# Kernel tuning notes

Measured on AMD Instinct MI355X. Metric: run time of the kernel, lower is better.

Reference implementation:

```python
import jax, jax.numpy as jnp
import numpy as np


def rotary_pos_emb(x):
    # x: [b, h, l, k]; interleaved rotary embedding (pairs are (0,1),(2,3),...)
    dim = x.shape[-1]
    seq = x.shape[-2]
    ts = jnp.arange(0, dim, 2, dtype=jnp.float32)
    inv_freqs = 10000.0 ** (-ts / dim)                      # [dim/2]
    grid = jnp.arange(seq, dtype=jnp.float32)[:, None] * inv_freqs[None, :]  # [l, dim/2]
    sin_embs = jnp.repeat(jnp.sin(grid), 2, axis=-1)[None]  # [1, l, dim] (interleaved repeat)
    cos_embs = jnp.repeat(jnp.cos(grid), 2, axis=-1)[None]
    x1, x2 = x[..., ::2], x[..., 1::2]
    xs = jnp.stack([-x2, x1], axis=-1).reshape(x.shape)     # interleave (-x2, x1)
    return x * cos_embs + xs * sin_embs


def setup_inputs() -> dict:
    key = jax.random.key(0)
    ks = jax.random.split(key, 5)
    b, l, d = 2, 2048, 1024
    scale = 1.0 / np.sqrt(d)
    return {
        "x": jax.random.normal(ks[0], (b, l, d), dtype=jnp.float32),
        "Wq": jax.random.normal(ks[1], (d, d), dtype=jnp.float32) * scale,
        "Wk": jax.random.normal(ks[2], (d, d), dtype=jnp.float32) * scale,
        "Wv": jax.random.normal(ks[3], (d, d), dtype=jnp.float32) * scale,
        "Wo": jax.random.normal(ks[4], (d, d), dtype=jnp.float32) * scale,
        "is_training": 0,
    }


def reference(x, Wq, Wk, Wv, Wo, is_training):
    n_heads = 16
    b, l, d = x.shape
    k_size = d // n_heads
    # NOTE: module scales q by 1/sqrt(model_size), not 1/sqrt(key_size)
    q = (x @ Wq) / jnp.sqrt(jnp.float32(d))
    q = q.reshape(b, l, n_heads, k_size).transpose(0, 2, 1, 3)  # b h l k
    k = (x @ Wk).reshape(b, l, n_heads, k_size).transpose(0, 2, 1, 3)
    v = (x @ Wv).reshape(b, l, n_heads, k_size).transpose(0, 2, 1, 3)
    q = rotary_pos_emb(q)
    k = rotary_pos_emb(k)
    logits = jnp.einsum('bhik,bhjk->bhij', q, k)  # no mask, no dropout (eval)
    a = jax.nn.softmax(logits, axis=-1)
    y = jnp.einsum('bhij,bhjv->bhiv', a, v)
    y = y.transpose(0, 2, 1, 3).reshape(b, l, d)  # b l (h v)
    return y @ Wo
```

## Files before the change

### kernel.cpp

```cpp
#include <hip/hip_runtime.h>
#include <stdint.h>

typedef unsigned short u16;
using short8 = __attribute__((ext_vector_type(8))) short;
using f32x4  = __attribute__((ext_vector_type(4))) float;

typedef __attribute__((address_space(1))) unsigned int gu32;
typedef __attribute__((address_space(3))) unsigned int lu32;

__device__ __forceinline__ void gl2lds16(const u16* g, u16* lds_wave_base) {
    __builtin_amdgcn_global_load_lds(
        (gu32*)(uintptr_t)(const void*)g,
        (lu32*)(uint32_t)(uintptr_t)(void*)lds_wave_base,
        16, 0, 0);
}

__device__ inline float bf2f(u16 u) {
    union { unsigned int i; float f; } v;
    v.i = ((unsigned int)u) << 16;
    return v.f;
}
__device__ inline u16 f2bf(float f) {
    union { float f; unsigned int i; } v;
    v.f = f;
    unsigned int x = v.i;
    return (u16)((x + 0x7fffu + ((x >> 16) & 1u)) >> 16);
}
__device__ inline u16 f2bf_trunc(float f) {
    union { float f; unsigned int i; } v;
    v.f = f;
    return (u16)(v.i >> 16);
}

__global__ __launch_bounds__(256) void cvt_x(const float* __restrict__ x,
                                             u16* __restrict__ xb)
{
    int i = (blockIdx.x * 256 + threadIdx.x) * 4;
    float4 v = *(const float4*)(x + i);
    ushort4 o;
    o.x = f2bf(v.x); o.y = f2bf(v.y); o.z = f2bf(v.z); o.w = f2bf(v.w);
    *(ushort4*)(xb + i) = o;
}

__global__ __launch_bounds__(256) void rope_tab(float2* __restrict__ tab)
{
    int idx = blockIdx.x * 256 + threadIdx.x;
    int pos = idx >> 5, pi = idx & 31;
    const float l2_10000_over_32 = 0.41524101186f;
    float ang = (float)pos * __builtin_amdgcn_exp2f(-(float)pi * l2_10000_over_32);
    float sn, cs;
    __sincosf(ang, &sn, &cs);
    tab[idx] = make_float2(cs, sn);
}

__global__ __launch_bounds__(256) void transpose4_cvt(
    const float* __restrict__ w0, const float* __restrict__ w1,
    const float* __restrict__ w2, const float* __restrict__ w3,
    u16* __restrict__ t0, u16* __restrict__ t1,
    u16* __restrict__ t2, u16* __restrict__ t3)
{
    __shared__ u16 tile[32][33];
    const float* src; u16* dst;
    switch (blockIdx.z) {
        case 0:  src = w0; dst = t0; break;
        case 1:  src = w1; dst = t1; break;
        case 2:  src = w2; dst = t2; break;
        default: src = w3; dst = t3; break;
    }
    int tx = threadIdx.x, ty = threadIdx.y;
    int c0 = blockIdx.x * 32, r0 = blockIdx.y * 32;
    #pragma unroll
    for (int i = 0; i < 4; i++)
        tile[ty + i * 8][tx] = f2bf(src[(size_t)(r0 + ty + i * 8) * 1024 + c0 + tx]);
    __syncthreads();
    #pragma unroll
    for (int i = 0; i < 4; i++)
        dst[(size_t)(c0 + ty + i * 8) * 1024 + r0 + tx] = tile[tx][ty + i * 8];
}

__global__ __launch_bounds__(256) void transpose_v(const u16* __restrict__ Vb,
                                                   u16* __restrict__ VT)
{
    __shared__ u16 t[32][33];
    int bh = blockIdx.z, b = bh >> 4, h = bh & 15;
    int p0 = blockIdx.x * 32, c0 = blockIdx.y * 32;
    int tx = threadIdx.x, ty = threadIdx.y;
    #pragma unroll
    for (int i = 0; i < 4; i++)
        t[ty + i * 8][tx] = Vb[(size_t)(b * 2048 + p0 + ty + i * 8) * 1024 + h * 64 + c0 + tx];
    __syncthreads();
    #pragma unroll
    for (int i = 0; i < 4; i++)
        VT[((size_t)bh * 64 + c0 + ty + i * 8) * 2048 + p0 + tx] = t[tx][ty + i * 8];
}

__global__ __launch_bounds__(256) void gemm_qkv(
    const u16* __restrict__ A, const u16* __restrict__ Bt,
    const float2* __restrict__ ropetab,
    u16* __restrict__ Qb, u16* __restrict__ Kb, u16* __restrict__ Vb)
{
    __shared__ __align__(16) u16 As[128 * 32];
    __shared__ __align__(16) u16 Bs[128 * 32];
    __shared__ float2 scs[128 * 33];

    const int tid  = threadIdx.x;
    const int lane = tid & 63;
    const int wid  = tid >> 6;
    const int quad = lane >> 4;
    const int l15  = lane & 15;
    const int wm   = wid >> 1, wn = wid & 1;

    const int m0 = blockIdx.y * 128;
    const int n0 = blockIdx.x * 128;
    const int mat = n0 >> 10;
    const int ln0 = n0 & 1023;
    u16* C = (mat == 0) ? Qb : (mat == 1 ? Kb : Vb);

    if (mat < 2) {
        int pos0 = m0 & 2047;
        #pragma unroll
        for (int t = 0; t < 16; t++) {
            int idx = t * 256 + tid;
            int rr = idx >> 5, pp = idx & 31;
            scs[rr * 33 + pp] = ropetab[(size_t)(pos0 + rr) * 32 + pp];
        }
    }

    f32x4 acc[4][4] = {};

    for (int k0 = 0; k0 < 1024; k0 += 32) {
        #pragma unroll
        for (int it = 0; it < 2; it++) {
            int c   = it * 256 + tid;
            int row = c >> 2;
            int col = ((c & 3) ^ (row & 3)) * 8;
            u16* lbA = &As[(size_t)(it * 256 + wid * 64) * 8];
            u16* lbB = &Bs[(size_t)(it * 256 + wid * 64) * 8];
            gl2lds16(&A [(size_t)(m0 + row) * 1024 + k0 + col], lbA);
            gl2lds16(&Bt[(size_t)(n0 + row) * 1024 + k0 + col], lbB);
        }
        __syncthreads();

        short8 a[4], b[4];
        #pragma unroll
        for (int i = 0; i < 4; i++) {
            int ra = wm * 64 + i * 16 + l15;
            int rb = wn * 64 + i * 16 + l15;
            a[i] = *(const short8*)(&As[ra * 32 + ((quad ^ (ra & 3)) * 8)]);
            b[i] = *(const short8*)(&Bs[rb * 32 + ((quad ^ (rb & 3)) * 8)]);
        }
        #pragma unroll
        for (int i = 0; i < 4; i++)
            #pragma unroll
            for (int j = 0; j < 4; j++)
                acc[i][j] = __builtin_amdgcn_mfma_f32_16x16x32_bf16(a[i], b[j], acc[i][j], 0, 0, 0);
        __syncthreads();
    }

    const float scale = (mat == 0) ? (0.03125f * 1.44269504f) : 1.0f;
    const bool do_rope = (mat < 2);
    const int odd = l15 & 1;

    #pragma unroll
    for (int i = 0; i < 4; i++)
        #pragma unroll
        for (int j = 0; j < 4; j++)
            #pragma unroll
            for (int r = 0; r < 4; r++) {
                int lrow = wm * 64 + i * 16 + quad * 4 + r;
                int col  = ln0 + wn * 64 + j * 16 + l15;
                float v = acc[i][j][r] * scale;
                float outv;
                if (do_rope) {
                    float vp = __shfl_xor(v, 1);
                    int pi   = (col & 63) >> 1;
                    float2 sc = scs[lrow * 33 + pi];
                    outv = odd ? (v * sc.x + vp * sc.y) : (v * sc.x - vp * sc.y);
                } else {
                    outv = v;
                }
                C[(size_t)(m0 + lrow) * 1024 + col] = f2bf(outv);
            }
}

__global__ __launch_bounds__(256) void gemm_out(
    const u16* __restrict__ A, const u16* __restrict__ Bt, float* __restrict__ C)
{
    __shared__ __align__(16) u16 As[128 * 32];
    __shared__ __align__(16) u16 Bs[128 * 32];

    const int tid  = threadIdx.x;
    const int lane = tid & 63;
    const int wid  = tid >> 6;
    const int quad = lane >> 4;
    const int l15  = lane & 15;
    const int wm   = wid >> 1, wn = wid & 1;

    const int m0 = blockIdx.y * 128;
    const int n0 = blockIdx.x * 128;

    f32x4 acc[4][4] = {};

    for (int k0 = 0; k0 < 1024; k0 += 32) {
        #pragma unroll
        for (int it = 0; it < 2; it++) {
            int c   = it * 256 + tid;
            int row = c >> 2;
            int col = ((c & 3) ^ (row & 3)) * 8;
            u16* lbA = &As[(size_t)(it * 256 + wid * 64) * 8];
            u16* lbB = &Bs[(size_t)(it * 256 + wid * 64) * 8];
            gl2lds16(&A [(size_t)(m0 + row) * 1024 + k0 + col], lbA);
            gl2lds16(&Bt[(size_t)(n0 + row) * 1024 + k0 + col], lbB);
        }
        __syncthreads();

        short8 a[4], b[4];
        #pragma unroll
        for (int i = 0; i < 4; i++) {
            int ra = wm * 64 + i * 16 + l15;
            int rb = wn * 64 + i * 16 + l15;
            a[i] = *(const short8*)(&As[ra * 32 + ((quad ^ (ra & 3)) * 8)]);
            b[i] = *(const short8*)(&Bs[rb * 32 + ((quad ^ (rb & 3)) * 8)]);
        }
        #pragma unroll
        for (int i = 0; i < 4; i++)
            #pragma unroll
            for (int j = 0; j < 4; j++)
                acc[i][j] = __builtin_amdgcn_mfma_f32_16x16x32_bf16(a[i], b[j], acc[i][j], 0, 0, 0);
        __syncthreads();
    }

    #pragma unroll
    for (int i = 0; i < 4; i++)
        #pragma unroll
        for (int j = 0; j < 4; j++)
            #pragma unroll
            for (int r = 0; r < 4; r++) {
                int row = m0 + wm * 64 + i * 16 + quad * 4 + r;
                int col = n0 + wn * 64 + j * 16 + l15;
                C[(size_t)row * 1024 + col] = acc[i][j][r];
            }
}

__global__ __launch_bounds__(512) void attn(
    const u16* __restrict__ Q, const u16* __restrict__ Kb,
    const u16* __restrict__ VT, u16* __restrict__ Y)
{
    __shared__ __align__(16) u16 Ks [128 * 64];
    __shared__ __align__(16) u16 VTs[64 * 128];
    __shared__ __align__(16) u16 Ps [8][16 * 64];

    const int tid  = threadIdx.x;
    const int lane = tid & 63, wid = tid >> 6;
    const int quad = lane >> 4, l15 = lane & 15;

    const int bh = blockIdx.x;
    const int qt = blockIdx.y;
    const int bb = bh >> 4, h = bh & 15;

    const size_t base = ((size_t)bb * 2048) * 1024 + (size_t)h * 64;

    short8 qf[2];
    {
        size_t qrow = (size_t)qt * 128 + wid * 16 + l15;
        const u16* qp = Q + base + qrow * 1024;
        qf[0] = *(const short8*)(qp + quad * 8);
        qf[1] = *(const short8*)(qp + 32 + quad * 8);
    }

    f32x4 o[4] = {};
    float l_r[4] = {0.f, 0.f, 0.f, 0.f};

    for (int j0 = 0; j0 < 2048; j0 += 128) {
        __syncthreads();
        #pragma unroll
        for (int it = 0; it < 2; it++) {
            int c = it * 512 + tid;
            int rk = c >> 3, ck = ((c & 7)  ^ (rk & 7))  * 8;
            int rv = c >> 4, cv = ((c & 15) ^ (rv & 15)) * 8;
            u16* lbK = &Ks [(size_t)(it * 512 + wid * 64) * 8];
            u16* lbV = &VTs[(size_t)(it * 512 + wid * 64) * 8];
            gl2lds16(&Kb[base + (size_t)(j0 + rk) * 1024 + ck], lbK);
            gl2lds16(&VT[((size_t)bh * 64 + rv) * 2048 + j0 + cv], lbV);
        }
        __syncthreads();

        f32x4 s[8];
        #pragma unroll
        for (int nt = 0; nt < 8; nt++) {
            int R = nt * 16 + l15;
            short8 k0 = *(const short8*)(&Ks[R * 64 + (( quad      ^ (R & 7)) * 8)]);
            short8 k1 = *(const short8*)(&Ks[R * 64 + (((quad + 4) ^ (R & 7)) * 8)]);
            f32x4 z = {};
            z = __builtin_amdgcn_mfma_f32_16x16x32_bf16(qf[0], k0, z, 0, 0, 0);
            z = __builtin_amdgcn_mfma_f32_16x16x32_bf16(qf[1], k1, z, 0, 0, 0);
            s[nt] = z;
        }

        #pragma unroll
        for (int hh = 0; hh < 2; hh++) {
            #pragma unroll
            for (int n4 = 0; n4 < 4; n4++) {
                int nt = hh * 4 + n4;
                #pragma unroll
                for (int r = 0; r < 4; r++) {
                    float p = __builtin_amdgcn_exp2f(s[nt][r]);
                    l_r[r] += p;
                    int m = quad * 4 + r;
                    int col = n4 * 16 + l15;
                    Ps[wid][m * 64 + (((col >> 3) ^ (m & 7)) * 8) + (col & 7)]
                        = f2bf_trunc(p);
                }
            }
            asm volatile("s_waitcnt lgkmcnt(0)" ::: "memory");

            short8 pa0 = *(const short8*)(&Ps[wid][l15 * 64 + (( quad      ^ (l15 & 7)) * 8)]);
            short8 pa1 = *(const short8*)(&Ps[wid][l15 * 64 + (((quad + 4) ^ (l15 & 7)) * 8)]);
            #pragma unroll
            for (int nt = 0; nt < 4; nt++) {
                int R = nt * 16 + l15;
                short8 vb0 = *(const short8*)(&VTs[R * 128 + (((hh * 8 + quad)     ^ (R & 15)) * 8)]);
                short8 vb1 = *(const short8*)(&VTs[R * 128 + (((hh * 8 + quad + 4) ^ (R & 15)) * 8)]);
                o[nt] = __builtin_amdgcn_mfma_f32_16x16x32_bf16(pa0, vb0, o[nt], 0, 0, 0);
                o[nt] = __builtin_amdgcn_mfma_f32_16x16x32_bf16(pa1, vb1, o[nt], 0, 0, 0);
            }
            asm volatile("" ::: "memory");
        }
    }

    #pragma unroll
    for (int r = 0; r < 4; r++) {
        l_r[r] += __shfl_xor(l_r[r], 1);
        l_r[r] += __shfl_xor(l_r[r], 2);
        l_r[r] += __shfl_xor(l_r[r], 4);
        l_r[r] += __shfl_xor(l_r[r], 8);
        l_r[r] = 1.0f / l_r[r];
    }

    size_t qrow0 = (size_t)qt * 128 + wid * 16;
    #pragma unroll
    for (int nt = 0; nt < 4; nt++)
        #pragma unroll
        for (int r = 0; r < 4; r++) {
            size_t row = qrow0 + quad * 4 + r;
            Y[base + row * 1024 + nt * 16 + l15] = f2bf(o[nt][r] * l_r[r]);
        }
}

extern "C" void kernel_launch(void* const* d_in, const int* in_sizes, int n_in,
                              void* d_out, int out_size, void* d_ws, size_t ws_size,
                              hipStream_t stream)
{
    const float* x  = (const float*)d_in[0];
    const float* Wq = (const float*)d_in[1];
    const float* Wk = (const float*)d_in[2];
    const float* Wv = (const float*)d_in[3];
    const float* Wo = (const float*)d_in[4];
    float* out = (float*)d_out;

    char* ws = (char*)d_ws;
    u16*    xb    = (u16*)   (ws + (0ull  << 20));
    u16*    WqkvT = (u16*)   (ws + (8ull  << 20));
    u16*    WoT   = (u16*)   (ws + (14ull << 20));
    u16*    Qb    = (u16*)   (ws + (16ull << 20));
    u16*    Kb    = (u16*)   (ws + (24ull << 20));
    u16*    Vb    = (u16*)   (ws + (32ull << 20));
    u16*    VTb   = (u16*)   (ws + (40ull << 20));
    u16*    Yb    = (u16*)   (ws + (48ull << 20));
    float2* tab   = (float2*)(ws + (56ull << 20));

    cvt_x<<<4096, 256, 0, stream>>>(x, xb);
    rope_tab<<<256, 256, 0, stream>>>(tab);
    transpose4_cvt<<<dim3(32, 32, 4), dim3(32, 8), 0, stream>>>(
        Wq, Wk, Wv, Wo,
        WqkvT, WqkvT + (1024ull * 1024), WqkvT + (2048ull * 1024), WoT);
    gemm_qkv<<<dim3(24, 32), 256, 0, stream>>>(xb, WqkvT, tab, Qb, Kb, Vb);
    transpose_v<<<dim3(64, 2, 32), dim3(32, 8), 0, stream>>>(Vb, VTb);
    attn<<<dim3(32, 16), 512, 0, stream>>>(Qb, Kb, VTb, Yb);
    gemm_out<<<dim3(8, 32), 256, 0, stream>>>(Yb, WoT, out);
}
```

Baseline: 205.8 us.

## Give each attention wave two query tiles and fold rope table into transpose

The attention kernel drops from 8 waves to 4 waves per block. Each wave now handles 32 query rows, so every K and V fragment read from LDS feeds two MFMAs, which halves LDS read traffic per FLOP but doubles the accumulator registers per wave. Separately, the rope sin/cos table is now computed inside the weight transpose kernel as an extra grid slice, which removes one kernel launch. The risk is lower occupancy and less latency hiding in attention.

```diff
diff --git a/kernel.cpp b/kernel.cpp
--- a/kernel.cpp
+++ b/kernel.cpp
@@ -42,23 +42,27 @@
     *(ushort4*)(xb + i) = o;
 }
 
-__global__ __launch_bounds__(256) void rope_tab(float2* __restrict__ tab)
-{
-    int idx = blockIdx.x * 256 + threadIdx.x;
-    int pos = idx >> 5, pi = idx & 31;
-    const float l2_10000_over_32 = 0.41524101186f;
-    float ang = (float)pos * __builtin_amdgcn_exp2f(-(float)pi * l2_10000_over_32);
-    float sn, cs;
-    __sincosf(ang, &sn, &cs);
-    tab[idx] = make_float2(cs, sn);
-}
-
 __global__ __launch_bounds__(256) void transpose4_cvt(
     const float* __restrict__ w0, const float* __restrict__ w1,
     const float* __restrict__ w2, const float* __restrict__ w3,
     u16* __restrict__ t0, u16* __restrict__ t1,
-    u16* __restrict__ t2, u16* __restrict__ t3)
-{
+    u16* __restrict__ t2, u16* __restrict__ t3,
+    float2* __restrict__ tab)
+{
+    int tx = threadIdx.x, ty = threadIdx.y;
+    if (blockIdx.z == 4) {
+        int idx = (blockIdx.y * 32 + blockIdx.x) * 256 + ty * 32 + tx;
+        if (idx < 65536) {
+            int pos = idx >> 5, pi = idx & 31;
+            const float l2_10000_over_32 = 0.41524101186f;
+            float ang = (float)pos *
+                __builtin_amdgcn_exp2f(-(float)pi * l2_10000_over_32);
+            float sn, cs;
+            __sincosf(ang, &sn, &cs);
+            tab[idx] = make_float2(cs, sn);
+        }
+        return;
+    }
     __shared__ u16 tile[32][33];
     const float* src; u16* dst;
     switch (blockIdx.z) {
@@ -67,7 +71,6 @@
         case 2:  src = w2; dst = t2; break;
         default: src = w3; dst = t3; break;
     }
-    int tx = threadIdx.x, ty = threadIdx.y;
     int c0 = blockIdx.x * 32, r0 = blockIdx.y * 32;
     #pragma unroll
     for (int i = 0; i < 4; i++)
@@ -242,7 +245,7 @@
             }
 }
 
-__global__ __launch_bounds__(512) void attn(
+__global__ __launch_bounds__(256) void attn(
     const u16* __restrict__ Q, const u16* __restrict__ Kb,
     const u16* __restrict__ VT, u16* __restrict__ Y)
 {
@@ -260,91 +263,110 @@
 
     const size_t base = ((size_t)bb * 2048) * 1024 + (size_t)h * 64;
 
-    short8 qf[2];
-    {
-        size_t qrow = (size_t)qt * 128 + wid * 16 + l15;
+    short8 qf[2][2];
+    #pragma unroll
+    for (int mi = 0; mi < 2; mi++) {
+        size_t qrow = (size_t)qt * 128 + wid * 32 + mi * 16 + l15;
         const u16* qp = Q + base + qrow * 1024;
-        qf[0] = *(const short8*)(qp + quad * 8);
-        qf[1] = *(const short8*)(qp + 32 + quad * 8);
-    }
-
-    f32x4 o[4] = {};
-    float l_r[4] = {0.f, 0.f, 0.f, 0.f};
+        qf[mi][0] = *(const short8*)(qp + quad * 8);
+        qf[mi][1] = *(const short8*)(qp + 32 + quad * 8);
+    }
+
+    f32x4 o[2][4] = {};
+    float l_r[2][4] = {};
 
     for (int j0 = 0; j0 < 2048; j0 += 128) {
         __syncthreads();
         #pragma unroll
-        for (int it = 0; it < 2; it++) {
-            int c = it * 512 + tid;
+        for (int it = 0; it < 4; it++) {
+            int c = it * 256 + tid;
             int rk = c >> 3, ck = ((c & 7)  ^ (rk & 7))  * 8;
             int rv = c >> 4, cv = ((c & 15) ^ (rv & 15)) * 8;
-            u16* lbK = &Ks [(size_t)(it * 512 + wid * 64) * 8];
-            u16* lbV = &VTs[(size_t)(it * 512 + wid * 64) * 8];
+            u16* lbK = &Ks [(size_t)(it * 256 + wid * 64) * 8];
+            u16* lbV = &VTs[(size_t)(it * 256 + wid * 64) * 8];
             gl2lds16(&Kb[base + (size_t)(j0 + rk) * 1024 + ck], lbK);
             gl2lds16(&VT[((size_t)bh * 64 + rv) * 2048 + j0 + cv], lbV);
         }
         __syncthreads();
 
-        f32x4 s[8];
+        f32x4 s[2][8];
         #pragma unroll
         for (int nt = 0; nt < 8; nt++) {
             int R = nt * 16 + l15;
             short8 k0 = *(const short8*)(&Ks[R * 64 + (( quad      ^ (R & 7)) * 8)]);
             short8 k1 = *(const short8*)(&Ks[R * 64 + (((quad + 4) ^ (R & 7)) * 8)]);
-            f32x4 z = {};
-            z = __builtin_amdgcn_mfma_f32_16x16x32_bf16(qf[0], k0, z, 0, 0, 0);
-            z = __builtin_amdgcn_mfma_f32_16x16x32_bf16(qf[1], k1, z, 0, 0, 0);
-            s[nt] = z;
+            #pragma unroll
+            for (int mi = 0; mi < 2; mi++) {
+                f32x4 z = {};
+                z = __builtin_amdgcn_mfma_f32_16x16x32_bf16(qf[mi][0], k0, z, 0, 0, 0);
+                z = __builtin_amdgcn_mfma_f32_16x16x32_bf16(qf[mi][1], k1, z, 0, 0, 0);
+                s[mi][nt] = z;
+            }
         }
 
         #pragma unroll
         for (int hh = 0; hh < 2; hh++) {
             #pragma unroll
-            for (int n4 = 0; n4 < 4; n4++) {
-                int nt = hh * 4 + n4;
+            for (int mi = 0; mi < 2; mi++)
                 #pragma unroll
-                for (int r = 0; r < 4; r++) {
-                    float p = __builtin_amdgcn_exp2f(s[nt][r]);
-                    l_r[r] += p;
-                    int m = quad * 4 + r;
-                    int col = n4 * 16 + l15;
-                    Ps[wid][m * 64 + (((col >> 3) ^ (m & 7)) * 8) + (col & 7)]
-                        = f2bf_trunc(p);
+                for (int n4 = 0; n4 < 4; n4++) {
+                    int nt = hh * 4 + n4;
+                    #pragma unroll
+                    for (int r = 0; r < 4; r++) {
+                        float p = __builtin_amdgcn_exp2f(s[mi][nt][r]);
+                        l_r[mi][r] += p;
+                        int m = quad * 4 + r;
+                        int col = n4 * 16 + l15;
+                        Ps[wid * 2 + mi][m * 64 + (((col >> 3) ^ (m & 7)) * 8) + (col & 7)]
+                            = f2bf_trunc(p);
+                    }
                 }
-            }
             asm volatile("s_waitcnt lgkmcnt(0)" ::: "memory");
 
-            short8 pa0 = *(const short8*)(&Ps[wid][l15 * 64 + (( quad      ^ (l15 & 7)) * 8)]);
-            short8 pa1 = *(const short8*)(&Ps[wid][l15 * 64 + (((quad + 4) ^ (l15 & 7)) * 8)]);
+            short8 pa[2][2];
+            #pragma unroll
+            for (int mi = 0; mi < 2; mi++) {
+                pa[mi][0] = *(const short8*)(&Ps[wid * 2 + mi][l15 * 64 + (( quad      ^ (l15 & 7)) * 8)]);
+                pa[mi][1] = *(const short8*)(&Ps[wid * 2 + mi][l15 * 64 + (((quad + 4) ^ (l15 & 7)) * 8)]);
+            }
             #pragma unroll
             for (int nt = 0; nt < 4; nt++) {
                 int R = nt * 16 + l15;
                 short8 vb0 = *(const short8*)(&VTs[R * 128 + (((hh * 8 + quad)     ^ (R & 15)) * 8)]);
                 short8 vb1 = *(const short8*)(&VTs[R * 128 + (((hh * 8 + quad + 4) ^ (R & 15)) * 8)]);
-                o[nt] = __builtin_amdgcn_mfma_f32_16x16x32_bf16(pa0, vb0, o[nt], 0, 0, 0);
-                o[nt] = __builtin_amdgcn_mfma_f32_16x16x32_bf16(pa1, vb1, o[nt], 0, 0, 0);
+                #pragma unroll
+                for (int mi = 0; mi < 2; mi++) {
+                    o[mi][nt] = __builtin_amdgcn_mfma_f32_16x16x32_bf16(pa[mi][0], vb0, o[mi][nt], 0, 0, 0);
+                    o[mi][nt] = __builtin_amdgcn_mfma_f32_16x16x32_bf16(pa[mi][1], vb1, o[mi][nt], 0, 0, 0);
+                }
             }
             asm volatile("" ::: "memory");
         }
     }
 
     #pragma unroll
-    for (int r = 0; r < 4; r++) {
-        l_r[r] += __shfl_xor(l_r[r], 1);
-        l_r[r] += __shfl_xor(l_r[r], 2);
-        l_r[r] += __shfl_xor(l_r[r], 4);
-        l_r[r] += __shfl_xor(l_r[r], 8);
-        l_r[r] = 1.0f / l_r[r];
-    }
-
-    size_t qrow0 = (size_t)qt * 128 + wid * 16;
-    #pragma unroll
-    for (int nt = 0; nt < 4; nt++)
+    for (int mi = 0; mi < 2; mi++)
         #pragma unroll
         for (int r = 0; r < 4; r++) {
-            size_t row = qrow0 + quad * 4 + r;
-            Y[base + row * 1024 + nt * 16 + l15] = f2bf(o[nt][r] * l_r[r]);
-        }
+            float v = l_r[mi][r];
+            v += __shfl_xor(v, 1);
+            v += __shfl_xor(v, 2);
+            v += __shfl_xor(v, 4);
+            v += __shfl_xor(v, 8);
+            l_r[mi][r] = 1.0f / v;
+        }
+
+    #pragma unroll
+    for (int mi = 0; mi < 2; mi++) {
+        size_t qrow0 = (size_t)qt * 128 + wid * 32 + mi * 16;
+        #pragma unroll
+        for (int nt = 0; nt < 4; nt++)
+            #pragma unroll
+            for (int r = 0; r < 4; r++) {
+                size_t row = qrow0 + quad * 4 + r;
+                Y[base + row * 1024 + nt * 16 + l15] = f2bf(o[mi][nt][r] * l_r[mi][r]);
+            }
+    }
 }
 
 extern "C" void kernel_launch(void* const* d_in, const int* in_sizes, int n_in,
@@ -370,12 +392,11 @@
     float2* tab   = (float2*)(ws + (56ull << 20));
 
     cvt_x<<<4096, 256, 0, stream>>>(x, xb);
-    rope_tab<<<256, 256, 0, stream>>>(tab);
-    transpose4_cvt<<<dim3(32, 32, 4), dim3(32, 8), 0, stream>>>(
+    transpose4_cvt<<<dim3(32, 32, 5), dim3(32, 8), 0, stream>>>(
         Wq, Wk, Wv, Wo,
-        WqkvT, WqkvT + (1024ull * 1024), WqkvT + (2048ull * 1024), WoT);
+        WqkvT, WqkvT + (1024ull * 1024), WqkvT + (2048ull * 1024), WoT, tab);
     gemm_qkv<<<dim3(24, 32), 256, 0, stream>>>(xb, WqkvT, tab, Qb, Kb, Vb);
     transpose_v<<<dim3(64, 2, 32), dim3(32, 8), 0, stream>>>(Vb, VTb);
-    attn<<<dim3(32, 16), 512, 0, stream>>>(Qb, Kb, VTb, Yb);
+    attn<<<dim3(32, 16), 256, 0, stream>>>(Qb, Kb, VTb, Yb);
     gemm_out<<<dim3(8, 32), 256, 0, stream>>>(Yb, WoT, out);
 }
```

Result: no change. 204.8 us (-0.5%).
